# Performance work log

Hardware: AMD Instinct MI355X
Metric: run time of the kernel (lower is better)

## Reference

```python
import jax, jax.numpy as jnp
import numpy as np

HIDDEN = 1024
INTER = 4096
NUM_EXPERTS = 8
TOP_K = 2


def setup_inputs() -> dict:
    key = jax.random.key(0)
    k1, k2, k3, k4 = jax.random.split(key, 4)
    hidden_states = jax.random.normal(k1, (4, 1024, HIDDEN), dtype=jnp.float32)
    gate_w = jax.random.normal(k2, (HIDDEN, NUM_EXPERTS), dtype=jnp.float32) * 0.02
    w1 = jax.random.normal(k3, (NUM_EXPERTS, HIDDEN, INTER), dtype=jnp.float32) * 0.02
    w2 = jax.random.normal(k4, (NUM_EXPERTS, INTER, HIDDEN), dtype=jnp.float32) * 0.02
    return {"hidden_states": hidden_states, "gate_w": gate_w, "w1": w1, "w2": w2}


def reference(hidden_states, gate_w, w1, w2):
    B, S, H = hidden_states.shape
    x = hidden_states.reshape(-1, H)                       # [T, H]
    T = x.shape[0]
    router_logits = x @ gate_w                             # [T, E]
    probs = jax.nn.softmax(router_logits.astype(jnp.float32), axis=-1)
    routing_weights, selected_experts = jax.lax.top_k(probs, TOP_K)  # [T, K]
    routing_weights = routing_weights / routing_weights.sum(-1, keepdims=True)
    routing_weights = routing_weights.astype(x.dtype)
    # combine[t, e] = sum_k rw[t, k] * (sel[t, k] == e)
    combine = jnp.zeros((T, NUM_EXPERTS), x.dtype).at[
        jnp.arange(T)[:, None], selected_experts
    ].add(routing_weights)
    # dense grouped MLP over all experts; zero combine weight drops unrouted pairs
    h1 = jax.nn.gelu(jnp.einsum('th,ehi->tei', x, w1), approximate=False)  # [T, E, I]
    y = jnp.einsum('tei,eih->teh', h1, w2)                 # [T, E, H]
    out = jnp.einsum('teh,te->th', y, combine)             # [T, H]
    return out.reshape(B, S, H), router_logits
```

## Files before the change

kernel.cpp:

```cpp
#include <hip/hip_runtime.h>
#include <hip/hip_bf16.h>
#include <math.h>

typedef unsigned short u16;
typedef unsigned int u32;
typedef __bf16 bf16x8 __attribute__((ext_vector_type(8)));
typedef float f32x4 __attribute__((ext_vector_type(4)));

#define T_TOK 4096
#define HID   1024
#define INTER 4096
#define NEXP  8

#define WS_NEEDED 209978368ull

__device__ __forceinline__ u16 f2bf(float f) {
    u32 u = __builtin_bit_cast(u32, f);
    u += 0x7FFFu + ((u >> 16) & 1u);
    return (u16)(u >> 16);
}

__device__ __forceinline__ void gl2lds16(const void* g, void* l) {
    __builtin_amdgcn_global_load_lds(
        (const __attribute__((address_space(1))) u32*)g,
        (__attribute__((address_space(3))) u32*)l, 16, 0, 0);
}

__device__ __forceinline__ float fast_gelu(float v) {
    float u2 = v * (-1.5957691216f - 0.0713548163f * v * v);
    return v / (1.0f + __expf(u2));
}

__global__ __launch_bounds__(256) void router_kernel(
    const float* __restrict__ x, const float* __restrict__ gw,
    float* __restrict__ logits, int* __restrict__ counts,
    int* __restrict__ tlist, float* __restrict__ wlist)
{
    const int lane = threadIdx.x & 63, wv = threadIdx.x >> 6;
    const int t = blockIdx.x * 4 + wv;
    const float* xr = x + (size_t)t * HID;
    float a[8] = {0.f,0.f,0.f,0.f,0.f,0.f,0.f,0.f};
    for (int h = lane; h < HID; h += 64) {
        float xv = xr[h];
        const float4* g4 = (const float4*)(gw + h * 8);
        float4 g0 = g4[0], g1 = g4[1];
        a[0] += xv * g0.x; a[1] += xv * g0.y; a[2] += xv * g0.z; a[3] += xv * g0.w;
        a[4] += xv * g1.x; a[5] += xv * g1.y; a[6] += xv * g1.z; a[7] += xv * g1.w;
    }
#pragma unroll
    for (int e = 0; e < 8; e++) {
        float v = a[e];
        for (int o = 32; o > 0; o >>= 1) v += __shfl_down(v, o, 64);
        a[e] = v;
    }
    if (lane == 0) {
#pragma unroll
        for (int e = 0; e < 8; e++) logits[(size_t)t * 8 + e] = a[e];
        int e1 = 0; float b1 = a[0];
        for (int e = 1; e < 8; e++) if (a[e] > b1) { b1 = a[e]; e1 = e; }
        int e2 = -1; float b2 = -1e30f;
        for (int e = 0; e < 8; e++) if (e != e1 && a[e] > b2) { b2 = a[e]; e2 = e; }
        float wa = 1.0f / (1.0f + expf(b2 - b1));
        float wb = 1.0f - wa;
        int p = atomicAdd(&counts[e1], 1);
        tlist[e1 * T_TOK + p] = t; wlist[e1 * T_TOK + p] = wa;
        p = atomicAdd(&counts[e2], 1);
        tlist[e2 * T_TOK + p] = t; wlist[e2 * T_TOK + p] = wb;
    }
}

__global__ void scan_kernel(const int* __restrict__ counts, int* __restrict__ offs)
{
    if (threadIdx.x == 0) {
        int s = 0;
        for (int e = 0; e < 8; e++) { offs[e] = s; s += counts[e]; }
    }
}

__global__ __launch_bounds__(256) void convert_x_kernel(
    const float* __restrict__ src, u16* __restrict__ dst)
{
    const int idx = (blockIdx.x * 256 + threadIdx.x) * 8;
    float4 f0 = *(const float4*)(src + idx);
    float4 f1 = *(const float4*)(src + idx + 4);
    uint4 o;
    o.x = (u32)f2bf(f0.x) | ((u32)f2bf(f0.y) << 16);
    o.y = (u32)f2bf(f0.z) | ((u32)f2bf(f0.w) << 16);
    o.z = (u32)f2bf(f1.x) | ((u32)f2bf(f1.y) << 16);
    o.w = (u32)f2bf(f1.z) | ((u32)f2bf(f1.w) << 16);
    *(uint4*)(dst + idx) = o;
}

__global__ __launch_bounds__(256) void transpose_convert_kernel(
    const float* __restrict__ src, u16* __restrict__ dst, int R, int C)
{
    __shared__ float tl[64][65];
    const int e = blockIdx.z;
    const int c0 = blockIdx.x * 64, r0 = blockIdx.y * 64;
    const float* s = src + (size_t)e * R * C + (size_t)r0 * C + c0;
    const int tid = threadIdx.x;
#pragma unroll
    for (int it = 0; it < 4; it++) {
        int idx = it * 256 + tid;
        int r = idx >> 4;
        int c4 = (idx & 15) * 4;
        float4 v = *(const float4*)(s + (size_t)r * C + c4);
        tl[c4 + 0][r] = v.x;
        tl[c4 + 1][r] = v.y;
        tl[c4 + 2][r] = v.z;
        tl[c4 + 3][r] = v.w;
    }
    __syncthreads();
    u16* d = dst + (size_t)e * C * R + (size_t)c0 * R + r0;
#pragma unroll
    for (int it = 0; it < 2; it++) {
        int idx = it * 256 + tid;
        int c = idx >> 3;
        int rg = (idx & 7) * 8;
        u32 o[4];
#pragma unroll
        for (int p = 0; p < 4; p++)
            o[p] = (u32)f2bf(tl[c][rg + 2 * p]) | ((u32)f2bf(tl[c][rg + 2 * p + 1]) << 16);
        *(uint4*)(d + (size_t)c * R + rg) = *(uint4*)o;
    }
}

__global__ __launch_bounds__(512, 1) void gemm1_kernel(
    const u16* __restrict__ xb, const u16* __restrict__ w1t,
    const int* __restrict__ counts, const int* __restrict__ offs,
    const int* __restrict__ tlist, u16* __restrict__ h1b)
{
    const int id = blockIdx.x;
    const int e  = id & 7;
    const int mt = (id >> 3) & 7;
    const int nt = id >> 6;
    const int cnt = counts[e];
    if (mt * 256 >= cnt) return;

    __shared__ __align__(16) u16 As[2][16384];
    __shared__ __align__(16) u16 Bs[2][16384];
    __shared__ int toks[256];

    const int tid = threadIdx.x, lane = tid & 63, wv = tid >> 6;
    if (tid < 256) toks[tid] = tlist[e * T_TOK + min(mt * 256 + tid, cnt - 1)];
    __syncthreads();

    const int sr = tid >> 3;
    const int sp = tid & 7;
    u32 abase[4], bbase[4];
    const u32 w1off = ((u32)e * INTER + (u32)nt * 256) * HID;
#pragma unroll
    for (int j = 0; j < 4; j++) {
        int m = j * 64 + sr;
        u32 rot = (u32)((sp - m) & 7) * 8;
        abase[j] = (u32)toks[m] * HID + rot;
        bbase[j] = w1off + (u32)m * HID + rot;
    }

    f32x4 acc[8][4] = {};
    const int wm = wv & 1, wn = wv >> 1;

    auto STAGE = [&](int buf, int k0) {
#pragma unroll
        for (int j = 0; j < 4; j++)
            gl2lds16(xb + abase[j] + k0, &As[buf][j * 4096 + wv * 512]);
#pragma unroll
        for (int j = 0; j < 4; j++)
            gl2lds16(w1t + bbase[j] + k0, &Bs[buf][j * 4096 + wv * 512]);
    };

    auto COMPUTE = [&](int buf) {
#pragma unroll
        for (int kk = 0; kk < 2; kk++) {
            bf16x8 a[8], b[4];
            const int jjb = kk * 4 + (lane >> 4);
#pragma unroll
            for (int i = 0; i < 8; i++) {
                int m = wm * 128 + i * 16 + (lane & 15);
                a[i] = *(const bf16x8*)&As[buf][m * 64 + ((jjb + m) & 7) * 8];
            }
#pragma unroll
            for (int j = 0; j < 4; j++) {
                int n = wn * 64 + j * 16 + (lane & 15);
                b[j] = *(const bf16x8*)&Bs[buf][n * 64 + ((jjb + n) & 7) * 8];
            }
#pragma unroll
            for (int i = 0; i < 8; i++)
#pragma unroll
                for (int j = 0; j < 4; j++)
                    acc[i][j] = __builtin_amdgcn_mfma_f32_16x16x32_bf16(
                        a[i], b[j], acc[i][j], 0, 0, 0);
        }
    };

    STAGE(0, 0);
    __syncthreads();
    int cur = 0;
#pragma unroll 1
    for (int kt = 1; kt < HID / 64; kt++) {
        STAGE(cur ^ 1, kt * 64);
        COMPUTE(cur);
        __syncthreads();
        cur ^= 1;
    }
    COMPUTE(cur);

    const int pb = offs[e] + mt * 256;
    const int rem = cnt - mt * 256;
    const bool full = (rem >= 256);
#pragma unroll
    for (int i = 0; i < 8; i++) {
        const int mb = wm * 128 + i * 16 + ((lane >> 4) << 2);
#pragma unroll
        for (int j = 0; j < 4; j++) {
            const int n = nt * 256 + wn * 64 + j * 16 + (lane & 15);
#pragma unroll
            for (int r = 0; r < 4; r++) {
                const int m = mb + r;
                if (full || m < rem)
                    h1b[(size_t)(pb + m) * INTER + n] = f2bf(fast_gelu(acc[i][j][r]));
            }
        }
    }
}

__global__ __launch_bounds__(512, 1) void gemm2_kernel(
    const u16* __restrict__ h1b, const u16* __restrict__ w2t,
    const int* __restrict__ counts, const int* __restrict__ offs,
    const int* __restrict__ tlist, const float* __restrict__ wlist,
    float* __restrict__ out)
{
    const int id = blockIdx.x;
    const int e  = id & 7;
    const int mt = (id >> 3) & 7;
    const int nt = (id >> 6) & 3;
    const int ks = id >> 8;
    const int cnt = counts[e];
    if (mt * 256 >= cnt) return;

    __shared__ __align__(16) u16 As[2][16384];
    __shared__ __align__(16) u16 Bs[2][16384];
    __shared__ int toks[256];
    __shared__ float wgt[256];

    const int tid = threadIdx.x, lane = tid & 63, wv = tid >> 6;
    if (tid < 256) {
        int gi = e * T_TOK + min(mt * 256 + tid, cnt - 1);
        toks[tid] = tlist[gi];
        wgt[tid]  = wlist[gi];
    }
    __syncthreads();

    const int sr = tid >> 3;
    const int sp = tid & 7;
    u32 abase[4], bbase[4];
    const int prow = offs[e];
#pragma unroll
    for (int j = 0; j < 4; j++) {
        int m = j * 64 + sr;
        u32 rot = (u32)((sp - m) & 7) * 8;
        int row = prow + min(mt * 256 + m, cnt - 1);
        abase[j] = (u32)row * INTER + rot;
        bbase[j] = ((u32)e * HID + (u32)nt * 256 + (u32)m) * INTER + rot;
    }

    f32x4 acc[8][4] = {};
    const int wm = wv & 1, wn = wv >> 1;

    auto STAGE = [&](int buf, int k0) {
#pragma unroll
        for (int j = 0; j < 4; j++)
            gl2lds16(h1b + abase[j] + k0, &As[buf][j * 4096 + wv * 512]);
#pragma unroll
        for (int j = 0; j < 4; j++)
            gl2lds16(w2t + bbase[j] + k0, &Bs[buf][j * 4096 + wv * 512]);
    };

    auto COMPUTE = [&](int buf) {
#pragma unroll
        for (int kk = 0; kk < 2; kk++) {
            bf16x8 a[8], b[4];
            const int jjb = kk * 4 + (lane >> 4);
#pragma unroll
            for (int i = 0; i < 8; i++) {
                int m = wm * 128 + i * 16 + (lane & 15);
                a[i] = *(const bf16x8*)&As[buf][m * 64 + ((jjb + m) & 7) * 8];
            }
#pragma unroll
            for (int j = 0; j < 4; j++) {
                int n = wn * 64 + j * 16 + (lane & 15);
                b[j] = *(const bf16x8*)&Bs[buf][n * 64 + ((jjb + n) & 7) * 8];
            }
#pragma unroll
            for (int i = 0; i < 8; i++)
#pragma unroll
                for (int j = 0; j < 4; j++)
                    acc[i][j] = __builtin_amdgcn_mfma_f32_16x16x32_bf16(
                        a[i], b[j], acc[i][j], 0, 0, 0);
        }
    };

    const u32 kbase = (u32)ks * (INTER / 2);
    STAGE(0, kbase);
    __syncthreads();
    int cur = 0;
#pragma unroll 1
    for (int kt = 1; kt < (INTER / 2) / 64; kt++) {
        STAGE(cur ^ 1, kbase + kt * 64);
        COMPUTE(cur);
        __syncthreads();
        cur ^= 1;
    }
    COMPUTE(cur);

    const int rem = cnt - mt * 256;
    const bool full = (rem >= 256);
#pragma unroll
    for (int i = 0; i < 8; i++) {
        const int mb = wm * 128 + i * 16 + ((lane >> 4) << 2);
#pragma unroll
        for (int j = 0; j < 4; j++) {
            const int n = nt * 256 + wn * 64 + j * 16 + (lane & 15);
#pragma unroll
            for (int r = 0; r < 4; r++) {
                const int m = mb + r;
                if (full || m < rem)
                    atomicAdd(&out[(size_t)toks[m] * HID + n], acc[i][j][r] * wgt[m]);
            }
        }
    }
}

extern "C" void kernel_launch(void* const* d_in, const int* in_sizes, int n_in,
                              void* d_out, int out_size, void* d_ws, size_t ws_size,
                              hipStream_t stream)
{
    const float* x  = (const float*)d_in[0];
    const float* gw = (const float*)d_in[1];
    const float* w1 = (const float*)d_in[2];
    const float* w2 = (const float*)d_in[3];
    float* out    = (float*)d_out;
    float* logits = out + 4194304;

    char* ws = (char*)d_ws;
    int*   counts = (int*)ws;
    int*   offs   = (int*)(ws + 256);
    int*   tlist  = (int*)(ws + 1024);
    float* wlist  = (float*)(ws + 132096);
    u16*   xb     = (u16*)(ws + 263168);
    u16*   w1t    = (u16*)(ws + 8651776);
    u16*   w2t    = (u16*)(ws + 75760640);
    u16*   h1b    = (u16*)(ws + 142869504);

    if (ws_size < WS_NEEDED) return;

    hipMemsetAsync(out, 0, 4194304 * sizeof(float), stream);
    hipMemsetAsync(counts, 0, 256, stream);

    router_kernel<<<1024, 256, 0, stream>>>(x, gw, logits, counts, tlist, wlist);
    scan_kernel<<<1, 64, 0, stream>>>(counts, offs);
    convert_x_kernel<<<2048, 256, 0, stream>>>(x, xb);
    transpose_convert_kernel<<<dim3(64, 16, 8), 256, 0, stream>>>(w1, w1t, HID, INTER);
    transpose_convert_kernel<<<dim3(16, 64, 8), 256, 0, stream>>>(w2, w2t, INTER, HID);

    gemm1_kernel<<<1024, 512, 0, stream>>>(xb, w1t, counts, offs, tlist, h1b);
    gemm2_kernel<<<512, 512, 0, stream>>>(h1b, w2t, counts, offs, tlist, wlist, out);
}
```

Before: 758.7 us.

## Deepen GEMM pipelines to four-stage LDS ring with split K tiles and ping-pong barriers

Both expert GEMM kernels move from double-buffered 64-wide K tiles to a four-buffer ring of 32-wide K tiles, prefetched three stages ahead with explicit vmcnt waits. Each iteration splits its MFMA work into two halves, interleaving A and B loads between them, with s_barrier and s_setprio so that memory issue and matrix math from different waves overlap. The LDS swizzle is rewritten for the narrower row. This hides more global-load latency, at the cost of more barriers per K element and hand-counted vmcnt values that must exactly match the outstanding loads.

```diff
diff --git a/kernel.cpp b/kernel.cpp
--- a/kernel.cpp
+++ b/kernel.cpp
@@ -11,6 +11,7 @@
 #define HID   1024
 #define INTER 4096
 #define NEXP  8
+#define BK    32
 
 #define WS_NEEDED 209978368ull
 
@@ -125,6 +126,7 @@
     }
 }
 
+
 __global__ __launch_bounds__(512, 1) void gemm1_kernel(
     const u16* __restrict__ xb, const u16* __restrict__ w1t,
     const int* __restrict__ counts, const int* __restrict__ offs,
@@ -137,73 +139,103 @@
     const int cnt = counts[e];
     if (mt * 256 >= cnt) return;
 
-    __shared__ __align__(16) u16 As[2][16384];
-    __shared__ __align__(16) u16 Bs[2][16384];
+    __shared__ __align__(16) u16 AS[4][8192];
+    __shared__ __align__(16) u16 BS[4][8192];
     __shared__ int toks[256];
 
     const int tid = threadIdx.x, lane = tid & 63, wv = tid >> 6;
     if (tid < 256) toks[tid] = tlist[e * T_TOK + min(mt * 256 + tid, cnt - 1)];
     __syncthreads();
 
-    const int sr = tid >> 3;
-    const int sp = tid & 7;
-    u32 abase[4], bbase[4];
-    const u32 w1off = ((u32)e * INTER + (u32)nt * 256) * HID;
+    u32 gA[2], gB[2];
+    {
+        const u32 w1off = ((u32)e * INTER + (u32)nt * 256) * HID;
+#pragma unroll
+        for (int jj = 0; jj < 2; jj++) {
+            int m = jj * 128 + (tid >> 2);
+            u32 q = (u32)(((tid & 3) - (m >> 1)) & 3);
+            gA[jj] = (u32)toks[m] * HID + q * 8;
+            gB[jj] = w1off + (u32)m * HID + q * 8;
+        }
+    }
+    const u32 ldst = (u32)wv * 512;
+
+    const int wm = wv & 1, wn = wv >> 1;
+    u32 aoff[8], boff[4];
+#pragma unroll
+    for (int i = 0; i < 8; i++) {
+        int m = wm * 128 + i * 16 + (lane & 15);
+        aoff[i] = (u32)m * 32 + (u32)((((lane >> 4) + (m >> 1)) & 3) * 8);
+    }
 #pragma unroll
     for (int j = 0; j < 4; j++) {
-        int m = j * 64 + sr;
-        u32 rot = (u32)((sp - m) & 7) * 8;
-        abase[j] = (u32)toks[m] * HID + rot;
-        bbase[j] = w1off + (u32)m * HID + rot;
+        int n = wn * 64 + j * 16 + (lane & 15);
+        boff[j] = (u32)n * 32 + (u32)((((lane >> 4) + (n >> 1)) & 3) * 8);
     }
 
     f32x4 acc[8][4] = {};
-    const int wm = wv & 1, wn = wv >> 1;
-
-    auto STAGE = [&](int buf, int k0) {
-#pragma unroll
-        for (int j = 0; j < 4; j++)
-            gl2lds16(xb + abase[j] + k0, &As[buf][j * 4096 + wv * 512]);
-#pragma unroll
-        for (int j = 0; j < 4; j++)
-            gl2lds16(w1t + bbase[j] + k0, &Bs[buf][j * 4096 + wv * 512]);
-    };
-
-    auto COMPUTE = [&](int buf) {
-#pragma unroll
-        for (int kk = 0; kk < 2; kk++) {
-            bf16x8 a[8], b[4];
-            const int jjb = kk * 4 + (lane >> 4);
-#pragma unroll
-            for (int i = 0; i < 8; i++) {
-                int m = wm * 128 + i * 16 + (lane & 15);
-                a[i] = *(const bf16x8*)&As[buf][m * 64 + ((jjb + m) & 7) * 8];
-            }
-#pragma unroll
-            for (int j = 0; j < 4; j++) {
-                int n = wn * 64 + j * 16 + (lane & 15);
-                b[j] = *(const bf16x8*)&Bs[buf][n * 64 + ((jjb + n) & 7) * 8];
-            }
-#pragma unroll
-            for (int i = 0; i < 8; i++)
-#pragma unroll
-                for (int j = 0; j < 4; j++)
-                    acc[i][j] = __builtin_amdgcn_mfma_f32_16x16x32_bf16(
-                        a[i], b[j], acc[i][j], 0, 0, 0);
-        }
-    };
-
-    STAGE(0, 0);
-    __syncthreads();
-    int cur = 0;
+
+#pragma unroll
+    for (int p = 0; p < 3; p++) {
+        gl2lds16(xb + gA[0] + p * BK, &AS[p][ldst]);
+        gl2lds16(xb + gA[1] + p * BK, &AS[p][4096 + ldst]);
+        gl2lds16(w1t + gB[0] + p * BK, &BS[p][ldst]);
+        gl2lds16(w1t + gB[1] + p * BK, &BS[p][4096 + ldst]);
+    }
+    asm volatile("s_waitcnt vmcnt(8)" ::: "memory");
+    __builtin_amdgcn_s_barrier();
+    asm volatile("" ::: "memory");
+
+    const int NT = HID / BK;
 #pragma unroll 1
-    for (int kt = 1; kt < HID / 64; kt++) {
-        STAGE(cur ^ 1, kt * 64);
-        COMPUTE(cur);
-        __syncthreads();
-        cur ^= 1;
-    }
-    COMPUTE(cur);
+    for (int t = 0; t < NT; ++t) {
+        const int buf = t & 3;
+        const int sbuf = (t + 3) & 3;
+        const u32 sk = (u32)(t + 3) * BK;
+        const bool do_stage = (t + 3 < NT);
+
+        bf16x8 a[8], b[4];
+        if (do_stage) {
+            gl2lds16(xb + gA[0] + sk, &AS[sbuf][ldst]);
+            gl2lds16(xb + gA[1] + sk, &AS[sbuf][4096 + ldst]);
+        }
+#pragma unroll
+        for (int j = 0; j < 4; j++) b[j] = *(const bf16x8*)&BS[buf][boff[j]];
+#pragma unroll
+        for (int i = 0; i < 4; i++) a[i] = *(const bf16x8*)&AS[buf][aoff[i]];
+        __builtin_amdgcn_s_barrier();
+        __builtin_amdgcn_s_setprio(1);
+#pragma unroll
+        for (int i = 0; i < 4; i++)
+#pragma unroll
+            for (int j = 0; j < 4; j++)
+                acc[i][j] = __builtin_amdgcn_mfma_f32_16x16x32_bf16(
+                    a[i], b[j], acc[i][j], 0, 0, 0);
+        __builtin_amdgcn_s_setprio(0);
+        __builtin_amdgcn_s_barrier();
+        if (do_stage) {
+            gl2lds16(w1t + gB[0] + sk, &BS[sbuf][ldst]);
+            gl2lds16(w1t + gB[1] + sk, &BS[sbuf][4096 + ldst]);
+        }
+#pragma unroll
+        for (int i = 4; i < 8; i++) a[i] = *(const bf16x8*)&AS[buf][aoff[i]];
+        __builtin_amdgcn_s_barrier();
+        __builtin_amdgcn_s_setprio(1);
+#pragma unroll
+        for (int i = 4; i < 8; i++)
+#pragma unroll
+            for (int j = 0; j < 4; j++)
+                acc[i][j] = __builtin_amdgcn_mfma_f32_16x16x32_bf16(
+                    a[i], b[j], acc[i][j], 0, 0, 0);
+        __builtin_amdgcn_s_setprio(0);
+        if (t + 1 < NT) {
+            if (t + 3 < NT)      asm volatile("s_waitcnt vmcnt(8)" ::: "memory");
+            else if (t + 2 < NT) asm volatile("s_waitcnt vmcnt(4)" ::: "memory");
+            else                 asm volatile("s_waitcnt vmcnt(0)" ::: "memory");
+            __builtin_amdgcn_s_barrier();
+            asm volatile("" ::: "memory");
+        }
+    }
 
     const int pb = offs[e] + mt * 256;
     const int rem = cnt - mt * 256;
@@ -238,8 +270,8 @@
     const int cnt = counts[e];
     if (mt * 256 >= cnt) return;
 
-    __shared__ __align__(16) u16 As[2][16384];
-    __shared__ __align__(16) u16 Bs[2][16384];
+    __shared__ __align__(16) u16 AS[4][8192];
+    __shared__ __align__(16) u16 BS[4][8192];
     __shared__ int toks[256];
     __shared__ float wgt[256];
 
@@ -251,67 +283,97 @@
     }
     __syncthreads();
 
-    const int sr = tid >> 3;
-    const int sp = tid & 7;
-    u32 abase[4], bbase[4];
-    const int prow = offs[e];
+    const u32 kbase = (u32)ks * (INTER / 2);
+    u32 gA[2], gB[2];
+    {
+        const int prow = offs[e];
+#pragma unroll
+        for (int jj = 0; jj < 2; jj++) {
+            int m = jj * 128 + (tid >> 2);
+            u32 q = (u32)(((tid & 3) - (m >> 1)) & 3);
+            int row = prow + min(mt * 256 + m, cnt - 1);
+            gA[jj] = (u32)row * INTER + q * 8 + kbase;
+            gB[jj] = ((u32)e * HID + (u32)nt * 256 + (u32)m) * INTER + q * 8 + kbase;
+        }
+    }
+    const u32 ldst = (u32)wv * 512;
+
+    const int wm = wv & 1, wn = wv >> 1;
+    u32 aoff[8], boff[4];
+#pragma unroll
+    for (int i = 0; i < 8; i++) {
+        int m = wm * 128 + i * 16 + (lane & 15);
+        aoff[i] = (u32)m * 32 + (u32)((((lane >> 4) + (m >> 1)) & 3) * 8);
+    }
 #pragma unroll
     for (int j = 0; j < 4; j++) {
-        int m = j * 64 + sr;
-        u32 rot = (u32)((sp - m) & 7) * 8;
-        int row = prow + min(mt * 256 + m, cnt - 1);
-        abase[j] = (u32)row * INTER + rot;
-        bbase[j] = ((u32)e * HID + (u32)nt * 256 + (u32)m) * INTER + rot;
+        int n = wn * 64 + j * 16 + (lane & 15);
+        boff[j] = (u32)n * 32 + (u32)((((lane >> 4) + (n >> 1)) & 3) * 8);
     }
 
     f32x4 acc[8][4] = {};
-    const int wm = wv & 1, wn = wv >> 1;
-
-    auto STAGE = [&](int buf, int k0) {
-#pragma unroll
-        for (int j = 0; j < 4; j++)
-            gl2lds16(h1b + abase[j] + k0, &As[buf][j * 4096 + wv * 512]);
-#pragma unroll
-        for (int j = 0; j < 4; j++)
-            gl2lds16(w2t + bbase[j] + k0, &Bs[buf][j * 4096 + wv * 512]);
-    };
-
-    auto COMPUTE = [&](int buf) {
-#pragma unroll
-        for (int kk = 0; kk < 2; kk++) {
-            bf16x8 a[8], b[4];
-            const int jjb = kk * 4 + (lane >> 4);
-#pragma unroll
-            for (int i = 0; i < 8; i++) {
-                int m = wm * 128 + i * 16 + (lane & 15);
-                a[i] = *(const bf16x8*)&As[buf][m * 64 + ((jjb + m) & 7) * 8];
-            }
-#pragma unroll
-            for (int j = 0; j < 4; j++) {
-                int n = wn * 64 + j * 16 + (lane & 15);
-                b[j] = *(const bf16x8*)&Bs[buf][n * 64 + ((jjb + n) & 7) * 8];
-            }
-#pragma unroll
-            for (int i = 0; i < 8; i++)
-#pragma unroll
-                for (int j = 0; j < 4; j++)
-                    acc[i][j] = __builtin_amdgcn_mfma_f32_16x16x32_bf16(
-                        a[i], b[j], acc[i][j], 0, 0, 0);
-        }
-    };
-
-    const u32 kbase = (u32)ks * (INTER / 2);
-    STAGE(0, kbase);
-    __syncthreads();
-    int cur = 0;
+
+#pragma unroll
+    for (int p = 0; p < 3; p++) {
+        gl2lds16(h1b + gA[0] + p * BK, &AS[p][ldst]);
+        gl2lds16(h1b + gA[1] + p * BK, &AS[p][4096 + ldst]);
+        gl2lds16(w2t + gB[0] + p * BK, &BS[p][ldst]);
+        gl2lds16(w2t + gB[1] + p * BK, &BS[p][4096 + ldst]);
+    }
+    asm volatile("s_waitcnt vmcnt(8)" ::: "memory");
+    __builtin_amdgcn_s_barrier();
+    asm volatile("" ::: "memory");
+
+    const int NT = (INTER / 2) / BK;
 #pragma unroll 1
-    for (int kt = 1; kt < (INTER / 2) / 64; kt++) {
-        STAGE(cur ^ 1, kbase + kt * 64);
-        COMPUTE(cur);
-        __syncthreads();
-        cur ^= 1;
-    }
-    COMPUTE(cur);
+    for (int t = 0; t < NT; ++t) {
+        const int buf = t & 3;
+        const int sbuf = (t + 3) & 3;
+        const u32 sk = (u32)(t + 3) * BK;
+        const bool do_stage = (t + 3 < NT);
+
+        bf16x8 a[8], b[4];
+        if (do_stage) {
+            gl2lds16(h1b + gA[0] + sk, &AS[sbuf][ldst]);
+            gl2lds16(h1b + gA[1] + sk, &AS[sbuf][4096 + ldst]);
+        }
+#pragma unroll
+        for (int j = 0; j < 4; j++) b[j] = *(const bf16x8*)&BS[buf][boff[j]];
+#pragma unroll
+        for (int i = 0; i < 4; i++) a[i] = *(const bf16x8*)&AS[buf][aoff[i]];
+        __builtin_amdgcn_s_barrier();
+        __builtin_amdgcn_s_setprio(1);
+#pragma unroll
+        for (int i = 0; i < 4; i++)
+#pragma unroll
+            for (int j = 0; j < 4; j++)
+                acc[i][j] = __builtin_amdgcn_mfma_f32_16x16x32_bf16(
+                    a[i], b[j], acc[i][j], 0, 0, 0);
+        __builtin_amdgcn_s_setprio(0);
+        __builtin_amdgcn_s_barrier();
+        if (do_stage) {
+            gl2lds16(w2t + gB[0] + sk, &BS[sbuf][ldst]);
+            gl2lds16(w2t + gB[1] + sk, &BS[sbuf][4096 + ldst]);
+        }
+#pragma unroll
+        for (int i = 4; i < 8; i++) a[i] = *(const bf16x8*)&AS[buf][aoff[i]];
+        __builtin_amdgcn_s_barrier();
+        __builtin_amdgcn_s_setprio(1);
+#pragma unroll
+        for (int i = 4; i < 8; i++)
+#pragma unroll
+            for (int j = 0; j < 4; j++)
+                acc[i][j] = __builtin_amdgcn_mfma_f32_16x16x32_bf16(
+                    a[i], b[j], acc[i][j], 0, 0, 0);
+        __builtin_amdgcn_s_setprio(0);
+        if (t + 1 < NT) {
+            if (t + 3 < NT)      asm volatile("s_waitcnt vmcnt(8)" ::: "memory");
+            else if (t + 2 < NT) asm volatile("s_waitcnt vmcnt(4)" ::: "memory");
+            else                 asm volatile("s_waitcnt vmcnt(0)" ::: "memory");
+            __builtin_amdgcn_s_barrier();
+            asm volatile("" ::: "memory");
+        }
+    }
 
     const int rem = cnt - mt * 256;
     const bool full = (rem >= 256);
```

Result: slower. 777.7 us (+2.5%).
